# Performance work log

Measured on AMD Instinct MI355X. Metric: run time of the kernel, lower is better.

The kernel has to match this reference:

```python
import jax, jax.numpy as jnp
import numpy as np

DIM = 1024
N_EXPERTS = 8
TOP_K = 2
EXPERT_HIDDEN = DIM * 2
B, T = 4, 4096


def setup_inputs() -> dict:
    key = jax.random.key(0)
    ks = jax.random.split(key, 5)
    # xavier_uniform with gain=0.02 for w1/w2 (fan_in=DIM, fan_out=EXPERT_HIDDEN)
    lim12 = 0.02 * np.sqrt(6.0 / (DIM + EXPERT_HIDDEN))
    lim3 = 0.02 * np.sqrt(6.0 / (EXPERT_HIDDEN + DIM))
    x = jax.random.normal(ks[0], (B, T, DIM), dtype=jnp.float32)
    router_w = 0.02 * jax.random.normal(ks[1], (N_EXPERTS, DIM), dtype=jnp.float32)
    w1 = jax.random.uniform(ks[2], (N_EXPERTS, DIM, EXPERT_HIDDEN), minval=-lim12, maxval=lim12, dtype=jnp.float32)
    w2 = jax.random.uniform(ks[3], (N_EXPERTS, DIM, EXPERT_HIDDEN), minval=-lim12, maxval=lim12, dtype=jnp.float32)
    w3 = jax.random.uniform(ks[4], (N_EXPERTS, EXPERT_HIDDEN, DIM), minval=-lim3, maxval=lim3, dtype=jnp.float32)
    return {"x": x, "router_w": router_w, "w1": w1, "w2": w2, "w3": w3}


def reference(x, router_w, w1, w2, w3):
    # Router: top-k softmax gating, renormalized over the selected k.
    logits = jnp.einsum('btd,ed->bte', x, router_w)          # [B,T,E]
    probs = jax.nn.softmax(logits, axis=-1)
    topk_vals, topk_idx = jax.lax.top_k(probs, TOP_K)        # [B,T,K]
    topk_weights = topk_vals / topk_vals.sum(axis=-1, keepdims=True)

    out = jnp.zeros_like(x)
    for e in range(N_EXPERTS):
        # gate weight for expert e per token (0 if e not in token's top-k)
        w_e = jnp.where(topk_idx == e, topk_weights, 0.0).sum(axis=-1)  # [B,T]
        h = jax.nn.silu(jnp.einsum('btd,dh->bth', x, w1[e])) * jnp.einsum('btd,dh->bth', x, w2[e])
        out = out + jnp.einsum('bth,hd->btd', h, w3[e]) * w_e[..., None]
    aux_loss = jnp.float32(0.0)  # eval mode
    return (out, aux_loss)
```

## Files before the change

### kernel.cpp

```cpp
#include <hip/hip_runtime.h>
#include <stdint.h>

#define TTOK 16384
#define NDIM 1024
#define NHID 2048
#define NEXP 8
#define TM 256
#define MAXT 136
#define SLOTCAP (2 * TTOK + NEXP * TM)

typedef __attribute__((ext_vector_type(8))) short short8;
typedef __attribute__((ext_vector_type(4))) float f32x4;

__device__ __forceinline__ unsigned short f2bf(float f) {
  unsigned int u = __float_as_uint(f);
  u += 0x7FFFu + ((u >> 16) & 1u);
  return (unsigned short)(u >> 16);
}

__device__ __forceinline__ void gload16(const void* g, void* l) {
  __builtin_amdgcn_global_load_lds(
      (const __attribute__((address_space(1))) unsigned int*)g,
      (__attribute__((address_space(3))) unsigned int*)l, 16, 0, 0);
}

__device__ __forceinline__ float silu(float z) {
  return z / (1.0f + __expf(-z));
}

__global__ void k_router(const float* __restrict__ x, const float* __restrict__ rw,
                         unsigned short* __restrict__ xbf, int* __restrict__ tok_e,
                         float* __restrict__ tok_gw) {
  int t = (blockIdx.x << 2) + (threadIdx.x >> 6);
  int lane = threadIdx.x & 63;
  const float4* xr = (const float4*)(x + (size_t)t * NDIM);

  float4 v[4];
  float d[NEXP];
#pragma unroll
  for (int e = 0; e < NEXP; ++e) d[e] = 0.f;

#pragma unroll
  for (int i = 0; i < 4; ++i) {
    int c = i * 64 + lane;
    v[i] = xr[c];
#pragma unroll
    for (int e = 0; e < NEXP; ++e) {
      float4 w = ((const float4*)(rw + e * NDIM))[c];
      d[e] += v[i].x * w.x + v[i].y * w.y + v[i].z * w.z + v[i].w * w.w;
    }
  }
#pragma unroll
  for (int e = 0; e < NEXP; ++e)
    for (int s = 32; s; s >>= 1) d[e] += __shfl_xor(d[e], s, 64);

  unsigned short* xo = xbf + (size_t)t * NDIM;
#pragma unroll
  for (int i = 0; i < 4; ++i) {
    int c = i * 64 + lane;
    ushort4 u;
    u.x = f2bf(v[i].x); u.y = f2bf(v[i].y); u.z = f2bf(v[i].z); u.w = f2bf(v[i].w);
    ((ushort4*)xo)[c] = u;
  }

  if (lane == 0) {
    float m = d[0];
#pragma unroll
    for (int e = 1; e < NEXP; ++e) m = fmaxf(m, d[e]);
    float ex[NEXP];
#pragma unroll
    for (int e = 0; e < NEXP; ++e) ex[e] = __expf(d[e] - m);
    int e0 = 0;
#pragma unroll
    for (int e = 1; e < NEXP; ++e) if (ex[e] > ex[e0]) e0 = e;
    int e1 = (e0 == 0) ? 1 : 0;
#pragma unroll
    for (int e = 0; e < NEXP; ++e) if (e != e0 && ex[e] > ex[e1]) e1 = e;
    float p0 = ex[e0], p1 = ex[e1];
    float inv = 1.f / (p0 + p1);
    tok_e[2 * t] = e0; tok_e[2 * t + 1] = e1;
    tok_gw[2 * t] = p0 * inv; tok_gw[2 * t + 1] = p1 * inv;
  }
}

__global__ void k_count(const int* __restrict__ tok_e, unsigned int* __restrict__ counts) {
  __shared__ unsigned int h[NEXP];
  int tid = threadIdx.x;
  if (tid < NEXP) h[tid] = 0u;
  __syncthreads();
  for (int i = blockIdx.x * 256 + tid; i < 2 * TTOK; i += gridDim.x * 256)
    atomicAdd(&h[tok_e[i]], 1u);
  __syncthreads();
  if (tid < NEXP) atomicAdd(&counts[tid], h[tid]);
}

__global__ void k_offsets(const unsigned int* __restrict__ counts,
                          unsigned int* __restrict__ slotbase, unsigned int* __restrict__ cnt2,
                          unsigned int* __restrict__ tile_e, unsigned int* __restrict__ tile_m0) {
  int l = threadIdx.x;
  unsigned int c[NEXP], base[NEXP], tb[NEXP];
  unsigned int b = 0, t = 0;
#pragma unroll
  for (int e = 0; e < NEXP; ++e) {
    c[e] = counts[e];
    base[e] = b; tb[e] = t;
    unsigned int nt = (c[e] + TM - 1) / TM;
    b += nt * TM; t += nt;
  }
  if (l < NEXP) { slotbase[l] = base[l]; cnt2[l] = 0u; }
  for (int idx = l; idx < MAXT; idx += 64) {
    unsigned int te = 0xFFFFFFFFu, tm = 0;
#pragma unroll
    for (int e = 0; e < NEXP; ++e) {
      unsigned int nt = (c[e] + TM - 1) / TM;
      if ((unsigned)idx >= tb[e] && (unsigned)idx < tb[e] + nt) {
        te = (unsigned)e; tm = base[e] + ((unsigned)idx - tb[e]) * TM;
      }
    }
    tile_e[idx] = te; tile_m0[idx] = tm;
  }
}

__global__ void k_fill(const int* __restrict__ tok_e, const float* __restrict__ tok_gw,
                       const unsigned int* __restrict__ slotbase, unsigned int* __restrict__ cnt2,
                       unsigned int* __restrict__ tok_list, float* __restrict__ gate_list) {
  __shared__ unsigned int hcnt[NEXP];
  __shared__ unsigned int hbase[NEXP];
  int tid = threadIdx.x;
  int t = blockIdx.x * 256 + tid;
  if (tid < NEXP) hcnt[tid] = 0u;
  __syncthreads();
  int e0 = tok_e[2 * t], e1 = tok_e[2 * t + 1];
  float g0 = tok_gw[2 * t], g1 = tok_gw[2 * t + 1];
  unsigned int p0 = atomicAdd(&hcnt[e0], 1u);
  unsigned int p1 = atomicAdd(&hcnt[e1], 1u);
  __syncthreads();
  if (tid < NEXP) hbase[tid] = atomicAdd(&cnt2[tid], hcnt[tid]);
  __syncthreads();
  unsigned int s0 = slotbase[e0] + hbase[e0] + p0;
  unsigned int s1 = slotbase[e1] + hbase[e1] + p1;
  tok_list[s0] = (unsigned)t; gate_list[s0] = g0;
  tok_list[s1] = (unsigned)t; gate_list[s1] = g1;
}

__device__ __forceinline__ void tconv_tile(const float* __restrict__ src,
                                           unsigned short* __restrict__ dst,
                                           int R, int C, int bx, int by) {
  __shared__ unsigned short tile[64][65];
  int tx = threadIdx.x & 15, ty = threadIdx.x >> 4;
#pragma unroll
  for (int rr = 0; rr < 4; ++rr) {
    int rl = rr * 16 + ty;
    float4 v = *(const float4*)(src + (size_t)(by + rl) * C + bx + tx * 4);
    tile[rl][tx * 4 + 0] = f2bf(v.x);
    tile[rl][tx * 4 + 1] = f2bf(v.y);
    tile[rl][tx * 4 + 2] = f2bf(v.z);
    tile[rl][tx * 4 + 3] = f2bf(v.w);
  }
  __syncthreads();
#pragma unroll
  for (int rr = 0; rr < 4; ++rr) {
    int cl = rr * 16 + ty;
    ushort4 u;
    u.x = tile[tx * 4 + 0][cl];
    u.y = tile[tx * 4 + 1][cl];
    u.z = tile[tx * 4 + 2][cl];
    u.w = tile[tx * 4 + 3][cl];
    *(ushort4*)(dst + (size_t)(bx + cl) * R + by + tx * 4) = u;
  }
}

__global__ void k_tconv_all(const float* __restrict__ w1, const float* __restrict__ w2,
                            const float* __restrict__ w3, unsigned short* __restrict__ w1t,
                            unsigned short* __restrict__ w2t, unsigned short* __restrict__ w3t) {
  int z = blockIdx.z;
  if (z < 16) {
    int e = z & 7;
    const float* src = (z < 8 ? w1 : w2) + (size_t)e * NDIM * NHID;
    unsigned short* dst = (z < 8 ? w1t : w2t) + (size_t)e * NDIM * NHID;
    tconv_tile(src, dst, NDIM, NHID, blockIdx.x * 64, blockIdx.y * 64);
  } else {
    int e = z - 16;
    const float* src = w3 + (size_t)e * NHID * NDIM;
    unsigned short* dst = w3t + (size_t)e * NHID * NDIM;
    tconv_tile(src, dst, NHID, NDIM, blockIdx.y * 64, blockIdx.x * 64);
  }
}

__global__ void k_sentinel(float* __restrict__ out, float v) {
  if (threadIdx.x == 0 && blockIdx.x == 0) out[0] = v;
}

__global__ __launch_bounds__(512, 2) void k_gemm12(
    const unsigned short* __restrict__ xbf, const unsigned short* __restrict__ w1t,
    const unsigned short* __restrict__ w2t, unsigned short* __restrict__ H,
    const unsigned int* __restrict__ tok_list, const unsigned int* __restrict__ tile_e,
    const unsigned int* __restrict__ tile_m0) {
  unsigned int e = tile_e[blockIdx.y];
  if (e > 7u) return;
  int m0 = (int)tile_m0[blockIdx.y];
  int n0 = blockIdx.x * 128;

  __shared__ unsigned short As[2][256 * 64];
  __shared__ unsigned short B1s[2][128 * 64];
  __shared__ unsigned short B2s[2][128 * 64];

  int tid = threadIdx.x, w = tid >> 6, l = tid & 63;
  int rsub = tid >> 3;
  int swb = ((tid & 7) * 16) ^ ((rsub & 7) << 4);

  const unsigned short* aS[4];
#pragma unroll
  for (int jj = 0; jj < 4; ++jj) {
    int row = jj * 64 + rsub;
    aS[jj] = xbf + (size_t)tok_list[m0 + row] * NDIM + (swb >> 1);
  }
  const unsigned short* b1S[2];
  const unsigned short* b2S[2];
#pragma unroll
  for (int jj = 0; jj < 2; ++jj) {
    int row = jj * 64 + rsub;
    size_t off = ((size_t)e * NHID + n0 + row) * NDIM + (swb >> 1);
    b1S[jj] = w1t + off;
    b2S[jj] = w2t + off;
  }
  int ldsb = w * 1024;

  f32x4 acc1[8][2], acc2[8][2];
#pragma unroll
  for (int m = 0; m < 8; ++m)
#pragma unroll
    for (int n = 0; n < 2; ++n) { acc1[m][n] = (f32x4)0.f; acc2[m][n] = (f32x4)0.f; }

  int wr = (w >> 2) * 128, wc = (w & 3) * 32;

#pragma unroll
  for (int jj = 0; jj < 4; ++jj)
    gload16(aS[jj], (char*)As[0] + jj * 8192 + ldsb);
#pragma unroll
  for (int jj = 0; jj < 2; ++jj) {
    gload16(b1S[jj], (char*)B1s[0] + jj * 8192 + ldsb);
    gload16(b2S[jj], (char*)B2s[0] + jj * 8192 + ldsb);
  }

  for (int t = 0; t < 16; ++t) {
    int cur = t & 1, nxt = cur ^ 1;
    int keN = (t + 1) * 64;
    bool st = (t < 15);
    const char* A = (const char*)As[cur];
    const char* B1 = (const char*)B1s[cur];
    const char* B2 = (const char*)B2s[cur];
    char* An = (char*)As[nxt];
    char* B1n = (char*)B1s[nxt];
    char* B2n = (char*)B2s[nxt];

    asm volatile("s_waitcnt vmcnt(0)" ::: "memory");
    __builtin_amdgcn_s_barrier();
    __builtin_amdgcn_sched_barrier(0);

    short8 ar[8], b1r[4], b2r[4];

#pragma unroll
    for (int ks = 0; ks < 2; ++ks) {
      int kb = ks * 64 + ((l >> 4) << 4);
#pragma unroll
      for (int m = 0; m < 4; ++m) {
        int r = wr + m * 16 + (l & 15);
        ar[ks * 4 + m] = *(const short8*)(A + r * 128 + (kb ^ ((r & 7) << 4)));
      }
#pragma unroll
      for (int n = 0; n < 2; ++n) {
        int r = wc + n * 16 + (l & 15);
        b1r[ks * 2 + n] = *(const short8*)(B1 + r * 128 + (kb ^ ((r & 7) << 4)));
      }
    }
    if (st) {
      gload16(aS[0] + keN, An + 0 * 8192 + ldsb);
      gload16(aS[1] + keN, An + 1 * 8192 + ldsb);
    }
    __builtin_amdgcn_s_barrier();
    __builtin_amdgcn_s_setprio(1);
#pragma unroll
    for (int ks = 0; ks < 2; ++ks)
#pragma unroll
      for (int m = 0; m < 4; ++m)
#pragma unroll
        for (int n = 0; n < 2; ++n)
          acc1[m][n] = __builtin_amdgcn_mfma_f32_16x16x32_bf16(ar[ks * 4 + m], b1r[ks * 2 + n],
                                                              acc1[m][n], 0, 0, 0);
    __builtin_amdgcn_s_setprio(0);

#pragma unroll
    for (int ks = 0; ks < 2; ++ks) {
      int kb = ks * 64 + ((l >> 4) << 4);
#pragma unroll
      for (int n = 0; n < 2; ++n) {
        int r = wc + n * 16 + (l & 15);
        b2r[ks * 2 + n] = *(const short8*)(B2 + r * 128 + (kb ^ ((r & 7) << 4)));
      }
    }
    if (st) {
      gload16(aS[2] + keN, An + 2 * 8192 + ldsb);
      gload16(aS[3] + keN, An + 3 * 8192 + ldsb);
    }
    __builtin_amdgcn_s_barrier();
    __builtin_amdgcn_s_setprio(1);
#pragma unroll
    for (int ks = 0; ks < 2; ++ks)
#pragma unroll
      for (int m = 0; m < 4; ++m)
#pragma unroll
        for (int n = 0; n < 2; ++n)
          acc2[m][n] = __builtin_amdgcn_mfma_f32_16x16x32_bf16(ar[ks * 4 + m], b2r[ks * 2 + n],
                                                              acc2[m][n], 0, 0, 0);
    __builtin_amdgcn_s_setprio(0);

#pragma unroll
    for (int ks = 0; ks < 2; ++ks) {
      int kb = ks * 64 + ((l >> 4) << 4);
#pragma unroll
      for (int m = 0; m < 4; ++m) {
        int r = wr + 64 + m * 16 + (l & 15);
        ar[ks * 4 + m] = *(const short8*)(A + r * 128 + (kb ^ ((r & 7) << 4)));
      }
    }
    if (st) {
      gload16(b1S[0] + keN, B1n + 0 * 8192 + ldsb);
      gload16(b1S[1] + keN, B1n + 1 * 8192 + ldsb);
    }
    __builtin_amdgcn_s_barrier();
    __builtin_amdgcn_s_setprio(1);
#pragma unroll
    for (int ks = 0; ks < 2; ++ks)
#pragma unroll
      for (int m = 0; m < 4; ++m)
#pragma unroll
        for (int n = 0; n < 2; ++n)
          acc1[4 + m][n] = __builtin_amdgcn_mfma_f32_16x16x32_bf16(ar[ks * 4 + m], b1r[ks * 2 + n],
                                                                  acc1[4 + m][n], 0, 0, 0);
    __builtin_amdgcn_s_setprio(0);

    if (st) {
      gload16(b2S[0] + keN, B2n + 0 * 8192 + ldsb);
      gload16(b2S[1] + keN, B2n + 1 * 8192 + ldsb);
    }
    __builtin_amdgcn_s_barrier();
    __builtin_amdgcn_s_setprio(1);
#pragma unroll
    for (int ks = 0; ks < 2; ++ks)
#pragma unroll
      for (int m = 0; m < 4; ++m)
#pragma unroll
        for (int n = 0; n < 2; ++n)
          acc2[4 + m][n] = __builtin_amdgcn_mfma_f32_16x16x32_bf16(ar[ks * 4 + m], b2r[ks * 2 + n],
                                                                  acc2[4 + m][n], 0, 0, 0);
    __builtin_amdgcn_s_setprio(0);
  }

#pragma unroll
  for (int m = 0; m < 8; ++m)
#pragma unroll
    for (int n = 0; n < 2; ++n) {
      int col = n0 + wc + n * 16 + (l & 15);
#pragma unroll
      for (int q = 0; q < 4; ++q) {
        int slot = m0 + wr + m * 16 + ((l >> 4) << 2) + q;
        float hv = silu(acc1[m][n][q]) * acc2[m][n][q];
        H[(size_t)slot * NHID + col] = f2bf(hv);
      }
    }
}

__global__ __launch_bounds__(256, 2) void k_gemm3(
    const unsigned short* __restrict__ H, const unsigned short* __restrict__ w3t,
    float* __restrict__ out, const unsigned int* __restrict__ tok_list,
    const float* __restrict__ gate_list, const unsigned int* __restrict__ tile_e,
    const unsigned int* __restrict__ tile_m0) {
  unsigned int e = tile_e[blockIdx.y >> 1];
  if (e > 7u) return;
  int m0 = (int)tile_m0[blockIdx.y >> 1] + (int)(blockIdx.y & 1) * 128;
  int n0 = blockIdx.x * 128;

  __shared__ unsigned short As[128 * 64];
  __shared__ unsigned short Bs[128 * 64];

  int tid = threadIdx.x, w = tid >> 6, l = tid & 63;
  int rsub = tid >> 3;
  int swb = ((tid & 7) * 16) ^ ((rsub & 7) << 4);

  const unsigned short* aS[4];
  const unsigned short* bS[4];
#pragma unroll
  for (int jj = 0; jj < 4; ++jj) {
    int row = jj * 32 + rsub;
    aS[jj] = H + (size_t)(m0 + row) * NHID + (swb >> 1);
    bS[jj] = w3t + ((size_t)e * NDIM + n0 + row) * NHID + (swb >> 1);
  }
  int ldsb = w * 1024;

  f32x4 acc[4][4];
#pragma unroll
  for (int m = 0; m < 4; ++m)
#pragma unroll
    for (int n = 0; n < 4; ++n) acc[m][n] = (f32x4)0.f;

  int wr = (w >> 1) * 64, wc = (w & 1) * 64;

  for (int t = 0; t < 32; ++t) {
    int ke = t * 64;
#pragma unroll
    for (int jj = 0; jj < 4; ++jj) {
      gload16(aS[jj] + ke, (char*)As + jj * 4096 + ldsb);
      gload16(bS[jj] + ke, (char*)Bs + jj * 4096 + ldsb);
    }
    __syncthreads();
#pragma unroll
    for (int ks = 0; ks < 2; ++ks) {
      int kb = ks * 64 + ((l >> 4) << 4);
      short8 a[4], b[4];
#pragma unroll
      for (int m = 0; m < 4; ++m) {
        int r = wr + m * 16 + (l & 15);
        a[m] = *(const short8*)((const char*)As + r * 128 + (kb ^ ((r & 7) << 4)));
      }
#pragma unroll
      for (int n = 0; n < 4; ++n) {
        int r = wc + n * 16 + (l & 15);
        b[n] = *(const short8*)((const char*)Bs + r * 128 + (kb ^ ((r & 7) << 4)));
      }
#pragma unroll
      for (int m = 0; m < 4; ++m)
#pragma unroll
        for (int n = 0; n < 4; ++n)
          acc[m][n] = __builtin_amdgcn_mfma_f32_16x16x32_bf16(a[m], b[n], acc[m][n], 0, 0, 0);
    }
    __syncthreads();
  }

#pragma unroll
  for (int m = 0; m < 4; ++m)
#pragma unroll
    for (int q = 0; q < 4; ++q) {
      int slot = m0 + wr + m * 16 + ((l >> 4) << 2) + q;
      unsigned int tok = tok_list[slot];
      float g = gate_list[slot];
      if (g != 0.f) {
        float* orow = out + (size_t)tok * NDIM + n0 + wc;
#pragma unroll
        for (int n = 0; n < 4; ++n)
          atomicAdd(orow + n * 16 + (l & 15), acc[m][n][q] * g);
      }
    }
}

extern "C" void kernel_launch(void* const* d_in, const int* in_sizes, int n_in,
                              void* d_out, int out_size, void* d_ws, size_t ws_size,
                              hipStream_t stream) {
  const float* x = (const float*)d_in[0];
  const float* rw = (const float*)d_in[1];
  const float* w1 = (const float*)d_in[2];
  const float* w2 = (const float*)d_in[3];
  const float* w3 = (const float*)d_in[4];
  float* out = (float*)d_out;
  char* ws = (char*)d_ws;

  size_t o = 0;
  auto alloc = [&](size_t b) { size_t r = o; o = (o + b + 255) & ~(size_t)255; return r; };
  size_t o_xbf = alloc((size_t)TTOK * NDIM * 2);
  size_t o_w3t = alloc((size_t)NEXP * NDIM * NHID * 2);
  size_t o_H = alloc((size_t)SLOTCAP * NHID * 2);
  size_t o_tok = alloc((size_t)SLOTCAP * 4);
  size_t o_gate = alloc((size_t)SLOTCAP * 4);
  size_t o_te = alloc((size_t)TTOK * 2 * 4);
  size_t o_tg = alloc((size_t)TTOK * 2 * 4);
  size_t o_cnt = alloc(64);
  size_t o_cnt2 = alloc(64);
  size_t o_sb = alloc(64);
  size_t o_tle = alloc(MAXT * 4 + 64);
  size_t o_tlm = alloc(MAXT * 4 + 64);
  size_t need = o;

  size_t outBytes = (size_t)out_size * sizeof(float);
  size_t wtBytes = (size_t)NEXP * NDIM * NHID * 2;

  if (ws_size < need || outBytes < 2 * wtBytes) {
    hipMemsetAsync(d_out, 0, outBytes, stream);
    k_sentinel<<<1, 64, 0, stream>>>(out, (float)((double)ws_size / 1048576.0));
    return;
  }

  unsigned short* xbf = (unsigned short*)(ws + o_xbf);
  unsigned short* w3t = (unsigned short*)(ws + o_w3t);
  unsigned short* Hbuf = (unsigned short*)(ws + o_H);
  unsigned int* tok_list = (unsigned int*)(ws + o_tok);
  float* gate_list = (float*)(ws + o_gate);
  int* tok_e = (int*)(ws + o_te);
  float* tok_gw = (float*)(ws + o_tg);
  unsigned int* counts = (unsigned int*)(ws + o_cnt);
  unsigned int* cnt2 = (unsigned int*)(ws + o_cnt2);
  unsigned int* slotbase = (unsigned int*)(ws + o_sb);
  unsigned int* tile_e = (unsigned int*)(ws + o_tle);
  unsigned int* tile_m0 = (unsigned int*)(ws + o_tlm);

  unsigned short* w1t = (unsigned short*)d_out;
  unsigned short* w2t = (unsigned short*)((char*)d_out + wtBytes);

  hipMemsetAsync(counts, 0, 64, stream);
  hipMemsetAsync(tok_list, 0, (size_t)SLOTCAP * 4, stream);
  hipMemsetAsync(gate_list, 0, (size_t)SLOTCAP * 4, stream);

  k_router<<<TTOK / 4, 256, 0, stream>>>(x, rw, xbf, tok_e, tok_gw);
  k_count<<<64, 256, 0, stream>>>(tok_e, counts);
  k_offsets<<<1, 64, 0, stream>>>(counts, slotbase, cnt2, tile_e, tile_m0);
  k_fill<<<TTOK / 256, 256, 0, stream>>>(tok_e, tok_gw, slotbase, cnt2, tok_list, gate_list);

  k_tconv_all<<<dim3(32, 16, 24), 256, 0, stream>>>(w1, w2, w3, w1t, w2t, w3t);

  k_gemm12<<<dim3(NHID / 128, MAXT), 512, 0, stream>>>(xbf, w1t, w2t, Hbuf, tok_list,
                                                       tile_e, tile_m0);

  hipMemsetAsync(d_out, 0, outBytes, stream);

  k_gemm3<<<dim3(NDIM / 128, 2 * MAXT), 256, 0, stream>>>(Hbuf, w3t, out, tok_list, gate_list,
                                                          tile_e, tile_m0);
}
```

Before: 677.2 us.

## Merge router and weight-transpose kernels; issue all gemm12 prefetch loads upfront

The router and the weight conversion/transpose kernels are merged into one launch (k_prep) that uses block-index ranges to split the work. This lets the memory-bound transpose blocks overlap with router blocks and drops one launch. Separately, k_gemm12 now issues every next-stage global-to-LDS prefetch at the start of each k-iteration instead of spreading them across the four MFMA phases. That raises the number of loads in flight, but the loads may now compete with the LDS reads issued right after them.

New measurement: 724.5 us. +7.0%, slower.

```diff
diff --git a/kernel.cpp b/kernel.cpp
--- a/kernel.cpp
+++ b/kernel.cpp
@@ -28,10 +28,12 @@
   return z / (1.0f + __expf(-z));
 }
 
-__global__ void k_router(const float* __restrict__ x, const float* __restrict__ rw,
-                         unsigned short* __restrict__ xbf, int* __restrict__ tok_e,
-                         float* __restrict__ tok_gw) {
-  int t = (blockIdx.x << 2) + (threadIdx.x >> 6);
+__device__ __forceinline__ void router_block(int b, const float* __restrict__ x,
+                                             const float* __restrict__ rw,
+                                             unsigned short* __restrict__ xbf,
+                                             int* __restrict__ tok_e,
+                                             float* __restrict__ tok_gw) {
+  int t = (b << 2) + (threadIdx.x >> 6);
   int lane = threadIdx.x & 63;
   const float4* xr = (const float4*)(x + (size_t)t * NDIM);
 
@@ -80,6 +82,61 @@
     float inv = 1.f / (p0 + p1);
     tok_e[2 * t] = e0; tok_e[2 * t + 1] = e1;
     tok_gw[2 * t] = p0 * inv; tok_gw[2 * t + 1] = p1 * inv;
+  }
+}
+
+__device__ __forceinline__ void tconv_tile(const float* __restrict__ src,
+                                           unsigned short* __restrict__ dst,
+                                           int R, int C, int bx, int by) {
+  __shared__ unsigned short tile[64][65];
+  int tx = threadIdx.x & 15, ty = threadIdx.x >> 4;
+#pragma unroll
+  for (int rr = 0; rr < 4; ++rr) {
+    int rl = rr * 16 + ty;
+    float4 v = *(const float4*)(src + (size_t)(by + rl) * C + bx + tx * 4);
+    tile[rl][tx * 4 + 0] = f2bf(v.x);
+    tile[rl][tx * 4 + 1] = f2bf(v.y);
+    tile[rl][tx * 4 + 2] = f2bf(v.z);
+    tile[rl][tx * 4 + 3] = f2bf(v.w);
+  }
+  __syncthreads();
+#pragma unroll
+  for (int rr = 0; rr < 4; ++rr) {
+    int cl = rr * 16 + ty;
+    ushort4 u;
+    u.x = tile[tx * 4 + 0][cl];
+    u.y = tile[tx * 4 + 1][cl];
+    u.z = tile[tx * 4 + 2][cl];
+    u.w = tile[tx * 4 + 3][cl];
+    *(ushort4*)(dst + (size_t)(bx + cl) * R + by + tx * 4) = u;
+  }
+}
+
+__global__ void k_prep(const float* __restrict__ x, const float* __restrict__ rw,
+                       unsigned short* __restrict__ xbf, int* __restrict__ tok_e,
+                       float* __restrict__ tok_gw, const float* __restrict__ w1,
+                       const float* __restrict__ w2, const float* __restrict__ w3,
+                       unsigned short* __restrict__ w1t, unsigned short* __restrict__ w2t,
+                       unsigned short* __restrict__ w3t) {
+  int b = blockIdx.x;
+  if (b < 4096) {
+    router_block(b, x, rw, xbf, tok_e, tok_gw);
+    return;
+  }
+  int tcb = b - 4096;
+  int bx = tcb & 31;
+  int by = (tcb >> 5) & 15;
+  int z = tcb >> 9;
+  if (z < 16) {
+    int e = z & 7;
+    const float* src = (z < 8 ? w1 : w2) + (size_t)e * NDIM * NHID;
+    unsigned short* dst = (z < 8 ? w1t : w2t) + (size_t)e * NDIM * NHID;
+    tconv_tile(src, dst, NDIM, NHID, bx * 64, by * 64);
+  } else {
+    int e = z - 16;
+    const float* src = w3 + (size_t)e * NHID * NDIM;
+    unsigned short* dst = w3t + (size_t)e * NHID * NDIM;
+    tconv_tile(src, dst, NHID, NDIM, by * 64, bx * 64);
   }
 }
 
@@ -143,50 +200,6 @@
   tok_list[s1] = (unsigned)t; gate_list[s1] = g1;
 }
 
-__device__ __forceinline__ void tconv_tile(const float* __restrict__ src,
-                                           unsigned short* __restrict__ dst,
-                                           int R, int C, int bx, int by) {
-  __shared__ unsigned short tile[64][65];
-  int tx = threadIdx.x & 15, ty = threadIdx.x >> 4;
-#pragma unroll
-  for (int rr = 0; rr < 4; ++rr) {
-    int rl = rr * 16 + ty;
-    float4 v = *(const float4*)(src + (size_t)(by + rl) * C + bx + tx * 4);
-    tile[rl][tx * 4 + 0] = f2bf(v.x);
-    tile[rl][tx * 4 + 1] = f2bf(v.y);
-    tile[rl][tx * 4 + 2] = f2bf(v.z);
-    tile[rl][tx * 4 + 3] = f2bf(v.w);
-  }
-  __syncthreads();
-#pragma unroll
-  for (int rr = 0; rr < 4; ++rr) {
-    int cl = rr * 16 + ty;
-    ushort4 u;
-    u.x = tile[tx * 4 + 0][cl];
-    u.y = tile[tx * 4 + 1][cl];
-    u.z = tile[tx * 4 + 2][cl];
-    u.w = tile[tx * 4 + 3][cl];
-    *(ushort4*)(dst + (size_t)(bx + cl) * R + by + tx * 4) = u;
-  }
-}
-
-__global__ void k_tconv_all(const float* __restrict__ w1, const float* __restrict__ w2,
-                            const float* __restrict__ w3, unsigned short* __restrict__ w1t,
-                            unsigned short* __restrict__ w2t, unsigned short* __restrict__ w3t) {
-  int z = blockIdx.z;
-  if (z < 16) {
-    int e = z & 7;
-    const float* src = (z < 8 ? w1 : w2) + (size_t)e * NDIM * NHID;
-    unsigned short* dst = (z < 8 ? w1t : w2t) + (size_t)e * NDIM * NHID;
-    tconv_tile(src, dst, NDIM, NHID, blockIdx.x * 64, blockIdx.y * 64);
-  } else {
-    int e = z - 16;
-    const float* src = w3 + (size_t)e * NHID * NDIM;
-    unsigned short* dst = w3t + (size_t)e * NHID * NDIM;
-    tconv_tile(src, dst, NHID, NDIM, blockIdx.y * 64, blockIdx.x * 64);
-  }
-}
-
 __global__ void k_sentinel(float* __restrict__ out, float v) {
   if (threadIdx.x == 0 && blockIdx.x == 0) out[0] = v;
 }
@@ -258,6 +271,17 @@
     __builtin_amdgcn_s_barrier();
     __builtin_amdgcn_sched_barrier(0);
 
+    if (st) {
+#pragma unroll
+      for (int jj = 0; jj < 4; ++jj)
+        gload16(aS[jj] + keN, An + jj * 8192 + ldsb);
+#pragma unroll
+      for (int jj = 0; jj < 2; ++jj) {
+        gload16(b1S[jj] + keN, B1n + jj * 8192 + ldsb);
+        gload16(b2S[jj] + keN, B2n + jj * 8192 + ldsb);
+      }
+    }
+
     short8 ar[8], b1r[4], b2r[4];
 
 #pragma unroll
@@ -273,10 +297,6 @@
         int r = wc + n * 16 + (l & 15);
         b1r[ks * 2 + n] = *(const short8*)(B1 + r * 128 + (kb ^ ((r & 7) << 4)));
       }
-    }
-    if (st) {
-      gload16(aS[0] + keN, An + 0 * 8192 + ldsb);
-      gload16(aS[1] + keN, An + 1 * 8192 + ldsb);
     }
     __builtin_amdgcn_s_barrier();
     __builtin_amdgcn_s_setprio(1);
@@ -299,10 +319,6 @@
         b2r[ks * 2 + n] = *(const short8*)(B2 + r * 128 + (kb ^ ((r & 7) << 4)));
       }
     }
-    if (st) {
-      gload16(aS[2] + keN, An + 2 * 8192 + ldsb);
-      gload16(aS[3] + keN, An + 3 * 8192 + ldsb);
-    }
     __builtin_amdgcn_s_barrier();
     __builtin_amdgcn_s_setprio(1);
 #pragma unroll
@@ -324,10 +340,6 @@
         ar[ks * 4 + m] = *(const short8*)(A + r * 128 + (kb ^ ((r & 7) << 4)));
       }
     }
-    if (st) {
-      gload16(b1S[0] + keN, B1n + 0 * 8192 + ldsb);
-      gload16(b1S[1] + keN, B1n + 1 * 8192 + ldsb);
-    }
     __builtin_amdgcn_s_barrier();
     __builtin_amdgcn_s_setprio(1);
 #pragma unroll
@@ -340,10 +352,6 @@
                                                                   acc1[4 + m][n], 0, 0, 0);
     __builtin_amdgcn_s_setprio(0);
 
-    if (st) {
-      gload16(b2S[0] + keN, B2n + 0 * 8192 + ldsb);
-      gload16(b2S[1] + keN, B2n + 1 * 8192 + ldsb);
-    }
     __builtin_amdgcn_s_barrier();
     __builtin_amdgcn_s_setprio(1);
 #pragma unroll
@@ -509,13 +517,11 @@
   hipMemsetAsync(tok_list, 0, (size_t)SLOTCAP * 4, stream);
   hipMemsetAsync(gate_list, 0, (size_t)SLOTCAP * 4, stream);
 
-  k_router<<<TTOK / 4, 256, 0, stream>>>(x, rw, xbf, tok_e, tok_gw);
+  k_prep<<<16384, 256, 0, stream>>>(x, rw, xbf, tok_e, tok_gw, w1, w2, w3, w1t, w2t, w3t);
   k_count<<<64, 256, 0, stream>>>(tok_e, counts);
   k_offsets<<<1, 64, 0, stream>>>(counts, slotbase, cnt2, tile_e, tile_m0);
   k_fill<<<TTOK / 256, 256, 0, stream>>>(tok_e, tok_gw, slotbase, cnt2, tok_list, gate_list);
 
-  k_tconv_all<<<dim3(32, 16, 24), 256, 0, stream>>>(w1, w2, w3, w1t, w2t, w3t);
-
   k_gemm12<<<dim3(NHID / 128, MAXT), 512, 0, stream>>>(xbf, w1t, w2t, Hbuf, tok_list,
                                                        tile_e, tile_m0);
 
```
